# Kernel tuning notes

Measured on AMD Instinct MI355X. Metric: run time of the kernel, lower is better.

Reference implementation:

```python
import jax, jax.numpy as jnp
import numpy as np

B, H, N = 2, 4, 4096


def setup_inputs() -> dict:
    key = jax.random.key(0)
    ranking = jax.random.normal(key, (B, H, N, 1), dtype=jnp.float32)
    return {"ranking": ranking}


def reference(ranking):
    b_s, h, n = ranking.shape[:3]
    r = ranking[..., 0]  # [b, h, n]
    # stable descending argsort of ranking*100 (negate; jnp stable sort keeps tie order)
    sorted_idx = jnp.argsort(-r * 100.0, axis=2, stable=True)  # [b, h, n] int
    r_sort = jnp.take_along_axis(r, sorted_idx, axis=2)
    # rel_scaler = cumsum of ones = 1..n (no mask case)
    rel_scaler = jnp.cumsum(jnp.ones_like(r_sort), axis=2)
    rel_minus = jnp.cumsum(r_sort, axis=2)
    relative_ranking = rel_minus - rel_scaler * r_sort
    rel_scaler = jnp.maximum(rel_scaler - 1.0, 0.0)  # 0..n-1
    # Hrelu forward: hard ReLU (custom backward in torch; forward math is relu)
    rank = jax.nn.relu(relative_ranking)
    indicator = rel_scaler - rank
    indicator = jnp.where(indicator < 0, indicator + n, indicator)
    perm_value = jnp.exp(-indicator * 10.0)
    # sparse COO (bh, row, col) -> coalesce == scatter-add into dense [b*h, n, n]
    rows = rel_scaler.astype(jnp.int32).reshape(b_s * h, n)
    cols = sorted_idx.reshape(b_s * h, n).astype(jnp.int32)
    vals = perm_value.reshape(b_s * h, n)
    bh = jnp.arange(b_s * h, dtype=jnp.int32)[:, None]
    perm = jnp.zeros((b_s * h, n, n), jnp.float32).at[bh, rows, cols].add(vals)
    return perm
```

## Files before the change

### kernel.cpp

```cpp
#include <hip/hip_runtime.h>
#include <math.h>

#define N 4096
#define BH 8
#define THREADS 256
#define PARTS 32
#define EPB 128
#define EPT 4
#define SLICES 8
#define KPS (N / SLICES)
#define CHUNK (N / THREADS)
#define FILL_BLOCKS 4096
#define RPB (BH * N / FILL_BLOCKS)
#define BPR (N / RPB)

typedef float f32x4 __attribute__((ext_vector_type(4)));

__device__ __forceinline__ unsigned long long desc_key64(float r, int i) {
    float k = r * 100.0f;
    unsigned int b = __float_as_uint(k);
    unsigned int asc = (b & 0x80000000u) ? ~b : (b | 0x80000000u);
    return ((unsigned long long)(~asc) << 32) | (unsigned int)i;
}

__global__ __launch_bounds__(THREADS)
void rank_kernel(const float* __restrict__ ranking,
                 int* __restrict__ cols,
                 float* __restrict__ rsort) {
    __shared__ unsigned long long keys[N];
    __shared__ unsigned short partial[SLICES * EPB];

    const int bh   = blockIdx.x / PARTS;
    const int part = blockIdx.x % PARTS;
    const float* r = ranking + (size_t)bh * N;

    const float4* r4 = (const float4*)r;
    for (int i = threadIdx.x; i < N / 4; i += THREADS) {
        float4 w = r4[i];
        keys[i * 4 + 0] = desc_key64(w.x, i * 4 + 0);
        keys[i * 4 + 1] = desc_key64(w.y, i * 4 + 1);
        keys[i * 4 + 2] = desc_key64(w.z, i * 4 + 2);
        keys[i * 4 + 3] = desc_key64(w.w, i * 4 + 3);
    }
    __syncthreads();

    const int g = threadIdx.x & 31;
    const int s = threadIdx.x >> 5;
    const int e_base = g * EPT;

    unsigned long long mykey[EPT];
    #pragma unroll
    for (int j = 0; j < EPT; ++j)
        mykey[j] = keys[part * EPB + e_base + j];

    int cnt0 = 0, cnt1 = 0, cnt2 = 0, cnt3 = 0;
    const ulonglong2* k2 = (const ulonglong2*)(keys + s * KPS);
    #pragma unroll 4
    for (int k = 0; k < KPS / 2; ++k) {
        ulonglong2 kk = k2[k];
        cnt0 += (kk.x < mykey[0]) + (kk.y < mykey[0]);
        cnt1 += (kk.x < mykey[1]) + (kk.y < mykey[1]);
        cnt2 += (kk.x < mykey[2]) + (kk.y < mykey[2]);
        cnt3 += (kk.x < mykey[3]) + (kk.y < mykey[3]);
    }
    partial[s * EPB + e_base + 0] = (unsigned short)cnt0;
    partial[s * EPB + e_base + 1] = (unsigned short)cnt1;
    partial[s * EPB + e_base + 2] = (unsigned short)cnt2;
    partial[s * EPB + e_base + 3] = (unsigned short)cnt3;
    __syncthreads();

    if (threadIdx.x < EPB) {
        int rank = 0;
        #pragma unroll
        for (int t = 0; t < SLICES; ++t)
            rank += (int)partial[t * EPB + threadIdx.x];
        int e = part * EPB + threadIdx.x;
        size_t o = (size_t)bh * N + rank;
        cols[o]  = e;
        rsort[o] = r[e];
    }
}

__global__ __launch_bounds__(THREADS)
void scanfill_kernel(const int* __restrict__ cols,
                     const float* __restrict__ rsort,
                     float* __restrict__ out) {
    __shared__ double sdata[THREADS];
    __shared__ float  vals_l[RPB];

    const int tid = threadIdx.x;
    const int bh  = blockIdx.x / BPR;
    const int i0  = (blockIdx.x % BPR) * RPB;
    const size_t row0 = (size_t)bh * N + i0;
    const int t0  = i0 / CHUNK;

    int c[RPB];
    #pragma unroll
    for (int rr = 0; rr < RPB; ++rr) c[rr] = cols[row0 + rr];

    const float* rs = rsort + (size_t)bh * N;
    const int base = tid * CHUNK;
    float  v[CHUNK];
    double local[CHUNK];
    const float4* f4 = (const float4*)(rs + base);
    #pragma unroll
    for (int q = 0; q < CHUNK / 4; ++q) {
        float4 w = f4[q];
        v[q * 4 + 0] = w.x; v[q * 4 + 1] = w.y;
        v[q * 4 + 2] = w.z; v[q * 4 + 3] = w.w;
    }
    double ssum = 0.0;
    #pragma unroll
    for (int q = 0; q < CHUNK; ++q) { ssum += (double)v[q]; local[q] = ssum; }

    sdata[tid] = (tid < t0) ? ssum : 0.0;
    __syncthreads();
    #pragma unroll
    for (int s = THREADS / 2; s > 0; s >>= 1) {
        if (tid < s) sdata[tid] += sdata[tid + s];
        __syncthreads();
    }
    const double off = sdata[0];

    if (tid == t0) {
        #pragma unroll
        for (int rr = 0; rr < RPB; ++rr) {
            int i = i0 + rr;
            int q = i - base;
            double cumsum = off + local[q];
            double rel    = cumsum - (double)(i + 1) * (double)v[q];
            double rank   = rel > 0.0 ? rel : 0.0;
            double ind    = (double)i - rank;
            if (ind < 0.0) ind += (double)N;
            if (ind < 0.0) ind = 0.0;
            vals_l[rr] = (float)exp(ind * -10.0);
        }
    }
    __syncthreads();

    #pragma unroll
    for (int rr = 0; rr < RPB; ++rr) {
        f32x4* o = (f32x4*)(out + (row0 + rr) * (size_t)N);
        const int fc = c[rr] >> 2;
        const float vv = vals_l[rr];
        #pragma unroll
        for (int q = 0; q < 4; ++q) {
            int f = tid + THREADS * q;
            f32x4 w = {0.f, 0.f, 0.f, 0.f};
            if (f == fc) w[c[rr] & 3] = vv;
            __builtin_nontemporal_store(w, o + f);
        }
    }
}

extern "C" void kernel_launch(void* const* d_in, const int* in_sizes, int n_in,
                              void* d_out, int out_size, void* d_ws, size_t ws_size,
                              hipStream_t stream) {
    const float* ranking = (const float*)d_in[0];
    float* out = (float*)d_out;

    int*   cols  = (int*)d_ws;
    float* rsort = (float*)((char*)d_ws + sizeof(int) * (size_t)BH * N);

    rank_kernel<<<BH * PARTS, THREADS, 0, stream>>>(ranking, cols, rsort);
    scanfill_kernel<<<FILL_BLOCKS, THREADS, 0, stream>>>(cols, rsort, out);
}
```

Measured before the change: 536.7 us.

## Split dense fill into bulk zero kernel plus single-pass scan scatter

Replaces the per-row fill kernel, which recomputed the full prefix scan in every block, with a streaming zero-fill kernel followed by an 8-block kernel that does one block-wide scan per head and scatters the nonzero values. This removes the redundant scan work and conditional vector writes, leaving a pure bandwidth-bound zero fill. It adds a launch and a serialization dependency, and the scatter phase runs on only 8 blocks.

```diff
diff --git a/kernel.cpp b/kernel.cpp
--- a/kernel.cpp
+++ b/kernel.cpp
@@ -10,9 +10,8 @@
 #define SLICES 8
 #define KPS (N / SLICES)
 #define CHUNK (N / THREADS)
-#define FILL_BLOCKS 4096
-#define RPB (BH * N / FILL_BLOCKS)
-#define BPR (N / RPB)
+#define FILL_BLOCKS 2048
+#define FILL_ITERS 64
 
 typedef float f32x4 __attribute__((ext_vector_type(4)));
 
@@ -82,24 +81,38 @@
 }
 
 __global__ __launch_bounds__(THREADS)
-void scanfill_kernel(const int* __restrict__ cols,
-                     const float* __restrict__ rsort,
-                     float* __restrict__ out) {
+void zero_kernel(float* __restrict__ out) {
+    f32x4 z = {0.f, 0.f, 0.f, 0.f};
+    f32x4* o = (f32x4*)out;
+    size_t i = (size_t)blockIdx.x * THREADS + threadIdx.x;
+    const size_t stride = (size_t)FILL_BLOCKS * THREADS;
+    #pragma unroll 8
+    for (int k = 0; k < FILL_ITERS; ++k) {
+        __builtin_nontemporal_store(z, o + i);
+        i += stride;
+    }
+}
+
+__global__ __launch_bounds__(THREADS)
+void scanscatter_kernel(const int* __restrict__ cols,
+                        const float* __restrict__ rsort,
+                        float* __restrict__ out) {
     __shared__ double sdata[THREADS];
-    __shared__ float  vals_l[RPB];
 
-    const int tid = threadIdx.x;
-    const int bh  = blockIdx.x / BPR;
-    const int i0  = (blockIdx.x % BPR) * RPB;
-    const size_t row0 = (size_t)bh * N + i0;
-    const int t0  = i0 / CHUNK;
+    const int tid  = threadIdx.x;
+    const int bh   = blockIdx.x;
+    const int base = tid * CHUNK;
 
-    int c[RPB];
+    int c[CHUNK];
+    const int4* c4 = (const int4*)(cols + (size_t)bh * N + base);
     #pragma unroll
-    for (int rr = 0; rr < RPB; ++rr) c[rr] = cols[row0 + rr];
+    for (int q = 0; q < CHUNK / 4; ++q) {
+        int4 w = c4[q];
+        c[q * 4 + 0] = w.x; c[q * 4 + 1] = w.y;
+        c[q * 4 + 2] = w.z; c[q * 4 + 3] = w.w;
+    }
 
     const float* rs = rsort + (size_t)bh * N;
-    const int base = tid * CHUNK;
     float  v[CHUNK];
     double local[CHUNK];
     const float4* f4 = (const float4*)(rs + base);
@@ -113,43 +126,28 @@
     #pragma unroll
     for (int q = 0; q < CHUNK; ++q) { ssum += (double)v[q]; local[q] = ssum; }
 
-    sdata[tid] = (tid < t0) ? ssum : 0.0;
+    sdata[tid] = ssum;
     __syncthreads();
     #pragma unroll
-    for (int s = THREADS / 2; s > 0; s >>= 1) {
-        if (tid < s) sdata[tid] += sdata[tid + s];
+    for (int s = 1; s < THREADS; s <<= 1) {
+        double y = (tid >= s) ? sdata[tid - s] : 0.0;
+        __syncthreads();
+        sdata[tid] += y;
         __syncthreads();
     }
-    const double off = sdata[0];
+    const double off = sdata[tid] - ssum;
 
-    if (tid == t0) {
-        #pragma unroll
-        for (int rr = 0; rr < RPB; ++rr) {
-            int i = i0 + rr;
-            int q = i - base;
-            double cumsum = off + local[q];
-            double rel    = cumsum - (double)(i + 1) * (double)v[q];
-            double rank   = rel > 0.0 ? rel : 0.0;
-            double ind    = (double)i - rank;
-            if (ind < 0.0) ind += (double)N;
-            if (ind < 0.0) ind = 0.0;
-            vals_l[rr] = (float)exp(ind * -10.0);
-        }
-    }
-    __syncthreads();
-
+    float* obase = out + (size_t)bh * N * N;
     #pragma unroll
-    for (int rr = 0; rr < RPB; ++rr) {
-        f32x4* o = (f32x4*)(out + (row0 + rr) * (size_t)N);
-        const int fc = c[rr] >> 2;
-        const float vv = vals_l[rr];
-        #pragma unroll
-        for (int q = 0; q < 4; ++q) {
-            int f = tid + THREADS * q;
-            f32x4 w = {0.f, 0.f, 0.f, 0.f};
-            if (f == fc) w[c[rr] & 3] = vv;
-            __builtin_nontemporal_store(w, o + f);
-        }
+    for (int q = 0; q < CHUNK; ++q) {
+        int i = base + q;
+        double cumsum = off + local[q];
+        double rel    = cumsum - (double)(i + 1) * (double)v[q];
+        double rank   = rel > 0.0 ? rel : 0.0;
+        double ind    = (double)i - rank;
+        if (ind < 0.0) ind += (double)N;
+        if (ind < 0.0) ind = 0.0;
+        obase[(size_t)i * N + c[q]] = (float)exp(ind * -10.0);
     }
 }
 
@@ -163,5 +161,6 @@
     float* rsort = (float*)((char*)d_ws + sizeof(int) * (size_t)BH * N);
 
     rank_kernel<<<BH * PARTS, THREADS, 0, stream>>>(ranking, cols, rsort);
-    scanfill_kernel<<<FILL_BLOCKS, THREADS, 0, stream>>>(cols, rsort, out);
+    zero_kernel<<<FILL_BLOCKS, THREADS, 0, stream>>>(out);
+    scanscatter_kernel<<<BH, THREADS, 0, stream>>>(cols, rsort, out);
 }
```

Measured after the change: 576.4 us. +7.4%, slower.
